# Kernel optimization log

Measured on AMD Instinct MI355X. Metric: run time of the kernel, lower is better.

Reference implementation:

```python
import jax, jax.numpy as jnp
import numpy as np

N, E, O, C, D_IN, OUT, L, B = 10000, 80000, 10, 64, 16, 16, 2, 16
DEG, WIDEN, BD = 3, 4, 64
EPS = 1e-6


def fibonacci_sphere(n):
    # deterministic near-uniform grid of n unit vectors on S^2 (stands in for GridGenerator's repulsion grid)
    i = jnp.arange(n, dtype=jnp.float32) + 0.5
    phi = jnp.arccos(1.0 - 2.0 * i / n)
    theta = jnp.pi * (1.0 + 5.0 ** 0.5) * i
    return jnp.stack([jnp.cos(theta) * jnp.sin(phi), jnp.sin(theta) * jnp.sin(phi), jnp.cos(phi)], axis=-1)


def poly_features(x, degree):
    # PolynomialFeatures: concat x, x(x)x, x(x)x(x)x, ... flattened outer products
    feats = [x]
    cur = x
    for _ in range(degree):
        cur = (cur[..., :, None] * x[..., None, :]).reshape(x.shape[:-1] + (-1,))
        feats.append(cur)
    return jnp.concatenate(feats, axis=-1)


def layer_norm(x, scale, bias):
    mu = jnp.mean(x, axis=-1, keepdims=True)
    var = jnp.mean((x - mu) ** 2, axis=-1, keepdims=True)
    return (x - mu) * jax.lax.rsqrt(var + EPS) * scale + bias


def setup_inputs():
    key = jax.random.key(0)
    ks = jax.random.split(key, 16)
    def w(k, shape):
        return jax.random.normal(k, shape, dtype=jnp.float32) / np.sqrt(shape[-2])
    P_SP = 2 + 4 + 8 + 16  # poly features of 2-dim spatial invariants, degree 3
    P_OR = 4               # poly features of 1-dim orientation invariant, degree 3
    return {
        "x": jax.random.normal(ks[0], (N, D_IN), jnp.float32),
        "pos": jax.random.normal(ks[1], (N, 3), jnp.float32),
        "basis_w1": w(ks[2], (P_SP, C)), "basis_b1": jnp.zeros((C,), jnp.float32),
        "basis_w2": w(ks[3], (C, BD)), "basis_b2": jnp.zeros((BD,), jnp.float32),
        "fbasis_w1": w(ks[4], (P_OR, C)), "fbasis_b1": jnp.zeros((C,), jnp.float32),
        "fbasis_w2": w(ks[5], (C, BD)), "fbasis_b2": jnp.zeros((BD,), jnp.float32),
        "embed_w": w(ks[6], (D_IN, C)),
        "conv_kw": w(ks[7], (L, BD, C)),
        "conv_fw": w(ks[8], (L, BD, C)),
        "conv_b": jnp.zeros((L, C), jnp.float32),
        "norm_s": jnp.ones((L, C), jnp.float32),
        "norm_b": jnp.zeros((L, C), jnp.float32),
        "lin1_w": w(ks[9], (L, C, WIDEN * C)), "lin1_b": jnp.zeros((L, WIDEN * C), jnp.float32),
        "lin2_w": w(ks[10], (L, WIDEN * C, C)), "lin2_b": jnp.zeros((L, C), jnp.float32),
        "ro_w": w(ks[11], (L, C, OUT)), "ro_b": jnp.zeros((L, OUT), jnp.float32),
        "edge_index": jax.random.randint(ks[12], (2, E), 0, N, jnp.int32),
        "batch": jnp.sort(jax.random.randint(ks[13], (N,), 0, B, jnp.int32)),
    }


def reference(x, pos, basis_w1, basis_b1, basis_w2, basis_b2, fbasis_w1, fbasis_b1, fbasis_w2, fbasis_b2, embed_w, conv_kw, conv_fw, conv_b, norm_s, norm_b, lin1_w, lin1_b, lin2_w, lin2_b, ro_w, ro_b, edge_index, batch):
    ori = fibonacci_sphere(O)                                             # [O,3]
    send, recv = edge_index[0], edge_index[1]
    rel = (pos[send] - pos[recv])[:, None, :]                              # [E,1,3]
    inv1 = jnp.sum(rel * ori[None], axis=-1, keepdims=True)                # [E,O,1]
    inv2 = jnp.linalg.norm(rel - inv1 * ori[None], axis=-1, keepdims=True) # [E,O,1]
    inv3 = jnp.sum(ori[None, :, :] * ori[:, None, :], axis=-1, keepdims=True)  # [O,O,1]
    sp = jnp.concatenate([inv1, inv2], axis=-1)                            # [E,O,2]
    kb = jax.nn.gelu(poly_features(sp, DEG) @ basis_w1 + basis_b1)
    kb = jax.nn.gelu(kb @ basis_w2 + basis_b2)                             # [E,O,BD]
    fkb = jax.nn.gelu(poly_features(inv3, DEG) @ fbasis_w1 + fbasis_b1)
    fkb = jax.nn.gelu(fkb @ fbasis_w2 + fbasis_b2)                         # [O,O,BD]
    h = jnp.broadcast_to((x @ embed_w)[:, None, :], (N, O, C))             # [N,O,C]
    readout = jnp.zeros((N, O, OUT), h.dtype)
    for l in range(L):
        # depthwise spatial conv: gather-send, modulate by kernel, scatter-add to receivers
        msg = h[send] * (kb @ conv_kw[l])                                  # [E,O,C]
        h1 = jax.ops.segment_sum(msg, recv, num_segments=N)                # [N,O,C]
        # depthwise fiber (orientation) conv
        fk = fkb @ conv_fw[l]                                              # [O,O,C]
        h2 = jnp.einsum('noc,poc->npc', h1, fk) / O + conv_b[l]
        # ConvNeXt MLP + residual
        y = layer_norm(h2, norm_s[l], norm_b[l])
        y = jax.nn.gelu(y @ lin1_w[l] + lin1_b[l]) @ lin2_w[l] + lin2_b[l]
        h = h + y
        readout = readout + (h @ ro_w[l] + ro_b[l])
    readout = readout / L
    out_scalar = jnp.mean(readout, axis=-2)                                # [N,OUT]
    pooled = jnp.zeros((B, OUT), out_scalar.dtype).at[batch].add(out_scalar)
    return pooled
```

## Files before the change

### kernel.cpp

```cpp
#include <hip/hip_runtime.h>
#include <math.h>

#define N_   10000
#define E_   80000
#define O_   10
#define B_   16
#define OUT_ 16
#define NROW_ (N_*O_)
#define NITEM_ (E_*O_)

typedef __attribute__((ext_vector_type(8))) short bf16x8;
typedef __attribute__((ext_vector_type(4))) short bf16x4;
typedef __attribute__((ext_vector_type(4))) float f32x4;

#define MFMA16(a,b,c) __builtin_amdgcn_mfma_f32_16x16x32_bf16(a,b,c,0,0,0)

__device__ __forceinline__ float gelu_f(float x) {
    float u = fmaf(0.044715f, x * x, 1.0f);
    float e = __builtin_amdgcn_exp2f(2.3022083f * x * u);
    float r = __builtin_amdgcn_rcpf(e + 1.0f);
    return fmaf(-x, r, x);
}

__device__ __forceinline__ unsigned short f2bf(float f) {
    union { float f; unsigned int u; } v; v.f = f;
    unsigned int r = v.u + 0x7FFFu + ((v.u >> 16) & 1u);
    return (unsigned short)(r >> 16);
}
__device__ __forceinline__ float bf2f(unsigned short u) {
    union { unsigned int u; float f; } v; v.u = ((unsigned int)u) << 16;
    return v.f;
}
__device__ __forceinline__ unsigned int cvtpk(float lo, float hi) {
    unsigned int r;
    asm("v_cvt_pk_bf16_f32 %0, %1, %2" : "=v"(r) : "v"(lo), "v"(hi));
    return r;
}
__device__ __forceinline__ bf16x4 pack4(float a, float b, float c, float d) {
    union { unsigned int u[2]; bf16x4 v; } z;
    z.u[0] = cvtpk(a, b);
    z.u[1] = cvtpk(c, d);
    return z.v;
}

__device__ __forceinline__ void fib_vec(int idx, float& vx, float& vy, float& vz) {
    float i = (float)idx + 0.5f;
    float phi = acosf(1.0f - 2.0f * i / (float)O_);
    float theta = 3.14159265358979323846f * (1.0f + 2.2360679774997896964f) * i;
    float sp = sinf(phi);
    vx = cosf(theta) * sp; vy = sinf(theta) * sp; vz = cosf(phi);
}

__global__ __launch_bounds__(256) void k_pack(
    const float* __restrict__ bw1, const float* __restrict__ bw2,
    const float* __restrict__ ckw, const float* __restrict__ l1w,
    const float* __restrict__ l2w, const float* __restrict__ row_w,
    float* __restrict__ orig,
    unsigned short* __restrict__ wW1P, unsigned short* __restrict__ wW2P,
    unsigned short* __restrict__ wCKP, unsigned short* __restrict__ wL1P,
    unsigned short* __restrict__ wL2P, unsigned short* __restrict__ wROP)
{
    const int g = blockIdx.x * 256 + threadIdx.x;
    if (g < 2048) {
        int idx = g;
        int t = idx >> 9, rem = idx & 511;
        int ln = rem >> 3, j = rem & 7;
        int row = t*16 + (ln & 15);
        int k = (ln >> 4)*8 + j;
        float s = 0.0f;
        if (k < 14) {
            const int moff[14] = {0,1,2,3,5,6,7,10,13,14,15,19,25,29};
            const int mcnt[14] = {1,1,1,2,1,1,3,3,1,1,4,6,4,1};
            const int mlist[30] = {0,1,2,3,4,5,6,7,8,10,9,11,12,13,14,
                                   15,16,18,22,17,19,20,23,24,26,21,25,27,28,29};
            for (int q = 0; q < mcnt[k]; ++q) s += bw1[mlist[moff[k]+q]*64 + row];
        }
        wW1P[idx] = f2bf(s);
    } else if (g < 6144) {
        int idx = g - 2048;
        int t = idx >> 9, rem = idx & 511;
        int mt = t >> 1, ks = t & 1;
        int ln = rem >> 3, j = rem & 7;
        int row = mt*16 + (ln & 15);
        int k = ks*32 + (ln >> 4)*8 + j;
        wW2P[idx] = f2bf(bw2[k*64 + row]);
    } else if (g < 14336) {
        int idx = g - 6144;
        int l = idx >> 12, r2 = idx & 4095;
        int t = r2 >> 9, rem = r2 & 511;
        int mt = t >> 1, ks = t & 1;
        int ln = rem >> 3, j = rem & 7;
        int row = mt*16 + (ln & 15);
        int k = ks*32 + (ln >> 4)*8 + j;
        wCKP[idx] = f2bf(ckw[l*4096 + k*64 + row]);
    } else if (g < 47104) {
        int idx = g - 14336;
        int l = idx >> 14, r2 = idx & 16383;
        int t = r2 >> 9, rem = r2 & 511;
        int mt = t >> 1, ks = t & 1;
        int ln = rem >> 3, j = rem & 7;
        int row = mt*16 + (ln & 15);
        int k = ks*32 + (ln >> 4)*8 + j;
        wL1P[idx] = f2bf(l1w[l*16384 + k*256 + row]);
    } else if (g < 79872) {
        int idx = g - 47104;
        int l = idx >> 14, r2 = idx & 16383;
        int t = r2 >> 9, rem = r2 & 511;
        int mt2 = t >> 3, ksg = t & 7;
        int ln = rem >> 3, j = rem & 7;
        int row = mt2*16 + (ln & 15);
        int k = ksg*32 + (ln >> 4)*8 + j;
        wL2P[idx] = f2bf(l2w[l*16384 + k*64 + row]);
    } else if (g < 81920) {
        int idx = g - 79872;
        int l = idx >> 10, r2 = idx & 1023;
        int ks = r2 >> 9, rem = r2 & 511;
        int ln = rem >> 3, j = rem & 7;
        int row = ln & 15;
        int k = ks*32 + (ln >> 4)*8 + j;
        wROP[idx] = f2bf(row_w[l*1024 + k*16 + row]);
    } else if (g < 81920 + O_) {
        int o = g - 81920;
        float vx, vy, vz;
        fib_vec(o, vx, vy, vz);
        orig[o*3+0] = vx; orig[o*3+1] = vy; orig[o*3+2] = vz;
    }
}

__global__ __launch_bounds__(256) void k_fibpre(
    const float* __restrict__ fw1, const float* __restrict__ fb1,
    const float* __restrict__ fw2, const float* __restrict__ fb2,
    const float* __restrict__ cfw, float* __restrict__ fkg)
{
    __shared__ float sRow[4][64];
    const int wv = threadIdx.x >> 6, lane = threadIdx.x & 63;
    const int pr = blockIdx.x * 4 + wv;
    if (pr >= 100) return;
    const int i = pr / O_, j = pr % O_;
    float ix, iy, iz, jx, jy, jz;
    fib_vec(i, ix, iy, iz);
    fib_vec(j, jx, jy, jz);
    float a = ix*jx + iy*jy + iz*jz;
    float a2 = a*a, a3 = a2*a, a4 = a3*a;
    float v = fb1[lane];
    v = fmaf(a,  fw1[0*64+lane], v);
    v = fmaf(a2, fw1[1*64+lane], v);
    v = fmaf(a3, fw1[2*64+lane], v);
    v = fmaf(a4, fw1[3*64+lane], v);
    sRow[wv][lane] = gelu_f(v);
    float acc = fb2[lane];
    for (int b = 0; b < 64; ++b) acc = fmaf(sRow[wv][b], fw2[b*64+lane], acc);
    sRow[wv][lane] = gelu_f(acc);
    for (int l = 0; l < 2; ++l) {
        float s = 0.0f;
        for (int b = 0; b < 64; ++b) s = fmaf(sRow[wv][b], cfw[l*4096 + b*64 + lane], s);
        fkg[l*6400 + pr*64 + lane] = s;
    }
}

__global__ __launch_bounds__(256) void k_embed(
    const float* __restrict__ x, const float* __restrict__ ew,
    float* __restrict__ hg, unsigned short* __restrict__ hbf0)
{
    int t = blockIdx.x * 256 + threadIdx.x;
    if (t >= N_ * 64) return;
    int n = t >> 6, c = t & 63;
    float v = 0.0f;
#pragma unroll
    for (int k = 0; k < 16; ++k) v = fmaf(x[n*16+k], ew[k*64+c], v);
    int base = n * 640 + c;
#pragma unroll
    for (int o = 0; o < O_; ++o) hg[base + o*64] = v;
    hbf0[t] = f2bf(v);
}

__global__ __launch_bounds__(256) void k_hist(const int* __restrict__ ei, int* __restrict__ counts)
{
    int e = blockIdx.x * 256 + threadIdx.x;
    if (e < E_) atomicAdd(&counts[ei[E_ + e]], 1);
}

__global__ __launch_bounds__(1024) void k_scan(
    const int* __restrict__ counts, int* __restrict__ offs, int* __restrict__ cursor)
{
    __shared__ int part[1024];
    int t = threadIdx.x;
    const int CH = 10;
    int base_i = t * CH;
    int s = 0;
#pragma unroll
    for (int i = 0; i < CH; ++i) { int idx = base_i + i; if (idx < N_) s += counts[idx]; }
    part[t] = s;
    __syncthreads();
    for (int off = 1; off < 1024; off <<= 1) {
        int v = (t >= off) ? part[t - off] : 0;
        __syncthreads();
        part[t] += v;
        __syncthreads();
    }
    int run = (t > 0) ? part[t - 1] : 0;
#pragma unroll
    for (int i = 0; i < CH; ++i) {
        int idx = base_i + i;
        if (idx < N_) { offs[idx] = run; cursor[idx] = run; run += counts[idx]; }
    }
    if (t == 1023) offs[N_] = run;
}

__global__ __launch_bounds__(256) void k_scatter(
    const int* __restrict__ ei, const float* __restrict__ pos,
    int* __restrict__ cursor, int* __restrict__ csend, int* __restrict__ crecv,
    float* __restrict__ crel)
{
    int e = blockIdx.x * 256 + threadIdx.x;
    if (e >= E_) return;
    int s = ei[e], r = ei[E_ + e];
    int slot = atomicAdd(&cursor[r], 1);
    csend[slot] = s;
    crecv[slot] = r;
    crel[slot*3+0] = pos[s*3+0] - pos[r*3+0];
    crel[slot*3+1] = pos[s*3+1] - pos[r*3+1];
    crel[slot*3+2] = pos[s*3+2] - pos[r*3+2];
}

template<int KS, bool BIAS, bool GELU>
__device__ __forceinline__ void mfma_stageP(
    unsigned short* sData, const unsigned short* __restrict__ Wp,
    const float* __restrict__ bias, int rbase, int lane)
{
    const int lm = lane & 15, lk = lane >> 4;
    bf16x8 Bf[4][KS];
#pragma unroll
    for (int nt = 0; nt < 4; ++nt)
#pragma unroll
        for (int ks = 0; ks < KS; ++ks) {
            int r = rbase + nt*16 + lm;
            int kb = ks*64 + lk*16;
            Bf[nt][ks] = *(const bf16x8*)((const char*)sData + r*128 + (kb ^ ((r&7)<<4)));
        }
#pragma unroll
    for (int mt = 0; mt < 4; ++mt) {
        bf16x8 Af[KS];
#pragma unroll
        for (int ks = 0; ks < KS; ++ks)
            Af[ks] = *(const bf16x8*)(Wp + ((mt*KS + ks)*64 + lane)*8);
        f32x4 b4 = {0,0,0,0};
        if (BIAS) b4 = *(const f32x4*)(bias + mt*16 + (lk<<2));
#pragma unroll
        for (int nt = 0; nt < 4; ++nt) {
            f32x4 acc = b4;
#pragma unroll
            for (int ks = 0; ks < KS; ++ks) acc = MFMA16(Af[ks], Bf[nt][ks], acc);
            float v0 = acc[0], v1 = acc[1], v2 = acc[2], v3 = acc[3];
            if (GELU) { v0 = gelu_f(v0); v1 = gelu_f(v1); v2 = gelu_f(v2); v3 = gelu_f(v3); }
            bf16x4 pk = pack4(v0, v1, v2, v3);
            int rr = rbase + nt*16 + lm;
            int cb = mt*32 + (lk<<3);
            *(bf16x4*)((char*)sData + rr*128 + (cb ^ ((rr&7)<<4))) = pk;
        }
    }
}

template<bool L0>
__global__ __launch_bounds__(128) void k_msg(
    const unsigned short* __restrict__ hbf, float* __restrict__ h1g,
    const int* __restrict__ csend, const int* __restrict__ crecv,
    const float* __restrict__ crel, const float* __restrict__ ori,
    const unsigned short* __restrict__ wW1P, const unsigned short* __restrict__ wW2P,
    const unsigned short* __restrict__ wCKP_l,
    const float* __restrict__ bb1, const float* __restrict__ bb2)
{
    __shared__ unsigned short sData[128*64];
    const int tid = threadIdx.x;
    const int lane = tid & 63, wv = tid >> 6;
    const int item = blockIdx.x * 128 + tid;
    const int slot = item / 10;
    const int oo = item - slot * 10;
    const int snd = csend[slot];
    const int rcv = crecv[slot];
    {
        float r0 = crel[slot*3+0], r1 = crel[slot*3+1], r2 = crel[slot*3+2];
        float o0 = ori[oo*3+0], o1 = ori[oo*3+1], o2 = ori[oo*3+2];
        float a = r0*o0 + r1*o1 + r2*o2;
        float p0 = fmaf(-a, o0, r0), p1 = fmaf(-a, o1, r1), p2 = fmaf(-a, o2, r2);
        float b = sqrtf(p0*p0 + p1*p1 + p2*p2);
        float a2 = a*a, b2 = b*b, ab = a*b;
        float m[14];
        m[0]=a; m[1]=b; m[2]=a2; m[3]=ab; m[4]=b2;
        m[5]=a2*a; m[6]=a2*b; m[7]=a*b2; m[8]=b2*b;
        m[9]=a2*a2; m[10]=a2*ab; m[11]=a2*b2; m[12]=ab*b2; m[13]=b2*b2;
        unsigned int pk[16];
#pragma unroll
        for (int j = 0; j < 7; ++j) pk[j] = cvtpk(m[2*j], m[2*j+1]);
#pragma unroll
        for (int j = 7; j < 16; ++j) pk[j] = 0;
        int r = tid;
#pragma unroll
        for (int q = 0; q < 4; ++q) {
            int cb = q*16;
            *(f32x4*)((char*)sData + r*128 + (cb ^ ((r&7)<<4))) = ((const f32x4*)pk)[q];
        }
    }
    const int rbase = wv * 64;
    mfma_stageP<1, true,  true >(sData, wW1P,   bb1, rbase, lane);
    mfma_stageP<2, true,  true >(sData, wW2P,   bb2, rbase, lane);
    mfma_stageP<2, false, false>(sData, wCKP_l, (const float*)0, rbase, lane);

    const int myaddr = L0 ? (snd * 64) : ((snd * 10 + oo) * 64);
    int prevr = __shfl_up(rcv, 1);
    unsigned long long bmask = __ballot(lane > 0 && rcv != prevr);
    const unsigned short* hb = hbf + lane;
    float a0=0,a1c=0,a2c=0,a3c=0,a4c=0,a5c=0,a6c=0,a7c=0,a8c=0,a9c=0;
    int cur = __builtin_amdgcn_readfirstlane(rcv);
    int soi = (blockIdx.x * 128 + rbase) % 10;
#define FLUSH_RUN(R) { float* bp = h1g + (R)*640 + lane; \
    atomicAdd(bp+0,a0); atomicAdd(bp+64,a1c); atomicAdd(bp+128,a2c); atomicAdd(bp+192,a3c); \
    atomicAdd(bp+256,a4c); atomicAdd(bp+320,a5c); atomicAdd(bp+384,a6c); atomicAdd(bp+448,a7c); \
    atomicAdd(bp+512,a8c); atomicAdd(bp+576,a9c); \
    a0=a1c=a2c=a3c=a4c=a5c=a6c=a7c=a8c=a9c=0.0f; }
#pragma unroll
    for (int ch = 0; ch < 4; ++ch) {
        unsigned short hvu[16];
        float kcv[16];
#pragma unroll
        for (int j = 0; j < 16; ++j) {
            const int i = ch*16 + j;
            hvu[j] = hb[__builtin_amdgcn_readlane(myaddr, i)];
            const int rr = rbase + i;
            kcv[j] = bf2f(*(const unsigned short*)((const char*)sData + rr*128 + ((lane*2) ^ ((rr&7)<<4))));
        }
#pragma unroll
        for (int j = 0; j < 16; ++j) {
            const int i = ch*16 + j;
            if (bmask & (1ull << i)) { FLUSH_RUN(cur); cur = __builtin_amdgcn_readlane(rcv, i); }
            float mv = kcv[j] * bf2f(hvu[j]);
            if      (soi == 0) a0  += mv;
            else if (soi == 1) a1c += mv;
            else if (soi == 2) a2c += mv;
            else if (soi == 3) a3c += mv;
            else if (soi == 4) a4c += mv;
            else if (soi == 5) a5c += mv;
            else if (soi == 6) a6c += mv;
            else if (soi == 7) a7c += mv;
            else if (soi == 8) a8c += mv;
            else               a9c += mv;
            soi = (soi == 9) ? 0 : soi + 1;
        }
    }
    FLUSH_RUN(cur);
#undef FLUSH_RUN
}

__global__ __launch_bounds__(256) void k_fln(
    const float* __restrict__ h1, const float* __restrict__ fkg,
    const float* __restrict__ cb, const float* __restrict__ ns,
    const float* __restrict__ nb, unsigned short* __restrict__ y)
{
    __shared__ float sFK[6400];
    const int tid = threadIdx.x;
    for (int i = tid; i < 6400; i += 256) sFK[i] = fkg[i];
    __syncthreads();
    const int lane = tid & 63, wv = tid >> 6;
    float cbv = cb[lane], nsv = ns[lane], nbv = nb[lane];
    for (int g4 = blockIdx.x; g4 < N_/4; g4 += gridDim.x) {
        const int n = g4 * 4 + wv;
        float hr[10];
#pragma unroll
        for (int o = 0; o < O_; ++o) hr[o] = h1[n*640 + o*64 + lane];
#pragma unroll
        for (int p = 0; p < O_; ++p) {
            float v = 0.0f;
#pragma unroll
            for (int o = 0; o < O_; ++o) v = fmaf(hr[o], sFK[(p*O_+o)*64 + lane], v);
            v = v * 0.1f + cbv;
            float s = v, q = v*v;
#pragma unroll
            for (int d = 1; d < 64; d <<= 1) { s += __shfl_xor(s, d); q += __shfl_xor(q, d); }
            float mu = s * (1.0f/64.0f);
            float var = q * (1.0f/64.0f) - mu*mu;
            float rs = rsqrtf(var + 1e-6f);
            float yv = (v - mu) * rs * nsv + nbv;
            y[(n*O_ + p)*64 + lane] = f2bf(yv);
        }
    }
}

__global__ __launch_bounds__(256, 4) void k_mlp(
    unsigned short* ybuf, float* __restrict__ hg, float* __restrict__ rout,
    const unsigned short* __restrict__ wL1P_l, const float* __restrict__ l1b_l,
    const unsigned short* __restrict__ wL2P_l, const float* __restrict__ l2b_l,
    const unsigned short* __restrict__ wROP_l, const float* __restrict__ rob_l)
{
    __shared__ unsigned short sA[64*64];
    const int tid = threadIdx.x;
    const int lane = tid & 63, wv = tid >> 6;
    const int rb = blockIdx.x * 64;
#pragma unroll
    for (int i = tid*16; i < 64*128; i += 256*16) {
        int r = i >> 7, off = i & 127;
        int grow = rb + r; if (grow >= NROW_) grow = NROW_ - 1;
        *(f32x4*)((char*)sA + r*128 + (off ^ ((r&7)<<4))) =
            *(const f32x4*)((const char*)ybuf + (size_t)grow*128 + off);
    }
    __syncthreads();
    const int lm = lane & 15, lk = lane >> 4;
    const int r0 = wv*16 + lm;
    bf16x8 Yf[2];
#pragma unroll
    for (int ks = 0; ks < 2; ++ks) {
        int kb = ks*64 + lk*16;
        Yf[ks] = *(const bf16x8*)((const char*)sA + r0*128 + (kb ^ ((r0&7)<<4)));
    }
    f32x4 acc2[4];
#pragma unroll
    for (int m = 0; m < 4; ++m) acc2[m] = *(const f32x4*)(l2b_l + m*16 + (lk<<2));
#pragma unroll
    for (int jb = 0; jb < 4; ++jb) {
#pragma unroll
        for (int mt = 0; mt < 4; ++mt) {
            bf16x8 A1[2];
#pragma unroll
            for (int ks = 0; ks < 2; ++ks)
                A1[ks] = *(const bf16x8*)(wL1P_l + (((jb*4 + mt)*2 + ks)*64 + lane)*8);
            f32x4 acc = *(const f32x4*)(l1b_l + jb*64 + mt*16 + (lk<<2));
            acc = MFMA16(A1[0], Yf[0], acc);
            acc = MFMA16(A1[1], Yf[1], acc);
            bf16x4 pk = pack4(gelu_f(acc[0]), gelu_f(acc[1]), gelu_f(acc[2]), gelu_f(acc[3]));
            int cb = mt*32 + (lk<<3);
            *(bf16x4*)((char*)sA + r0*128 + (cb ^ ((r0&7)<<4))) = pk;
        }
        bf16x8 Mf[2];
#pragma unroll
        for (int ks = 0; ks < 2; ++ks) {
            int kb = ks*64 + lk*16;
            Mf[ks] = *(const bf16x8*)((const char*)sA + r0*128 + (kb ^ ((r0&7)<<4)));
        }
#pragma unroll
        for (int mt2 = 0; mt2 < 4; ++mt2) {
            bf16x8 A2[2];
#pragma unroll
            for (int ks = 0; ks < 2; ++ks)
                A2[ks] = *(const bf16x8*)(wL2P_l + ((mt2*8 + jb*2 + ks)*64 + lane)*8);
            acc2[mt2] = MFMA16(A2[0], Mf[0], acc2[mt2]);
            acc2[mt2] = MFMA16(A2[1], Mf[1], acc2[mt2]);
        }
    }
    const int grow = rb + r0;
    const bool valid = grow < NROW_;
    const int growc = valid ? grow : (NROW_ - 1);
#pragma unroll
    for (int mt2 = 0; mt2 < 4; ++mt2) {
        f32x4 hv = *(const f32x4*)(hg + (size_t)growc*64 + mt2*16 + (lk<<2));
        f32x4 hn;
#pragma unroll
        for (int r = 0; r < 4; ++r) hn[r] = hv[r] + acc2[mt2][r];
        bf16x4 pk = pack4(hn[0], hn[1], hn[2], hn[3]);
        if (valid) {
            *(f32x4*)(hg + (size_t)grow*64 + mt2*16 + (lk<<2)) = hn;
            *(bf16x4*)((char*)ybuf + (size_t)grow*128 + (mt2*16 + (lk<<2))*2) = pk;
        }
        int cb = mt2*32 + (lk<<3);
        *(bf16x4*)((char*)sA + r0*128 + (cb ^ ((r0&7)<<4))) = pk;
    }
    bf16x8 Ro[2];
#pragma unroll
    for (int ks = 0; ks < 2; ++ks)
        Ro[ks] = *(const bf16x8*)(wROP_l + (ks*64 + lane)*8);
    f32x4 r4 = *(const f32x4*)(rob_l + (lk<<2));
    bf16x8 Hf[2];
#pragma unroll
    for (int ks = 0; ks < 2; ++ks) {
        int kb = ks*64 + lk*16;
        Hf[ks] = *(const bf16x8*)((const char*)sA + r0*128 + (kb ^ ((r0&7)<<4)));
    }
    r4 = MFMA16(Ro[0], Hf[0], r4);
    r4 = MFMA16(Ro[1], Hf[1], r4);
    if (valid) *(f32x4*)(rout + (size_t)grow*16 + (lk<<2)) = r4;
}

__global__ __launch_bounds__(256) void k_pool(
    const float* __restrict__ r0, const float* __restrict__ r1,
    const int* __restrict__ batch, float* __restrict__ out)
{
    int t = blockIdx.x * 256 + threadIdx.x;
    if (t >= N_ * 16) return;
    int n = t >> 4, j = t & 15;
    float s = 0.0f;
#pragma unroll
    for (int p = 0; p < O_; ++p)
        s += r0[(n*O_ + p)*16 + j] + r1[(n*O_ + p)*16 + j];
    atomicAdd(&out[batch[n]*16 + j], s * (1.0f/20.0f));
}

extern "C" void kernel_launch(void* const* d_in, const int* in_sizes, int n_in,
                              void* d_out, int out_size, void* d_ws, size_t ws_size,
                              hipStream_t stream)
{
    const float* x    = (const float*)d_in[0];
    const float* pos  = (const float*)d_in[1];
    const float* bw1  = (const float*)d_in[2];
    const float* bb1  = (const float*)d_in[3];
    const float* bw2  = (const float*)d_in[4];
    const float* bb2  = (const float*)d_in[5];
    const float* fw1  = (const float*)d_in[6];
    const float* fb1  = (const float*)d_in[7];
    const float* fw2  = (const float*)d_in[8];
    const float* fb2  = (const float*)d_in[9];
    const float* embw = (const float*)d_in[10];
    const float* ckw  = (const float*)d_in[11];
    const float* cfw  = (const float*)d_in[12];
    const float* cb   = (const float*)d_in[13];
    const float* ns   = (const float*)d_in[14];
    const float* nbp  = (const float*)d_in[15];
    const float* l1w  = (const float*)d_in[16];
    const float* l1b  = (const float*)d_in[17];
    const float* l2w  = (const float*)d_in[18];
    const float* l2b  = (const float*)d_in[19];
    const float* row  = (const float*)d_in[20];
    const float* rob  = (const float*)d_in[21];
    const int*   ei   = (const int*)d_in[22];
    const int*   batch= (const int*)d_in[23];
    float* out = (float*)d_out;

    char* w = (char*)d_ws;
    size_t off = 0;
    auto alloc = [&](size_t bytes) -> char* {
        char* p = w + off; off += (bytes + 255) / 256 * 256; return p;
    };
    float* ori    = (float*)alloc(32 * 4);
    float* fkg    = (float*)alloc(2 * 6400 * 4);
    unsigned short* wW1P = (unsigned short*)alloc(4*512*2);
    unsigned short* wW2P = (unsigned short*)alloc(8*512*2);
    unsigned short* wCKP = (unsigned short*)alloc(2*8*512*2);
    unsigned short* wL1P = (unsigned short*)alloc(2*32*512*2);
    unsigned short* wL2P = (unsigned short*)alloc(2*32*512*2);
    unsigned short* wROP = (unsigned short*)alloc(2*2*512*2);
    float* h      = (float*)alloc((size_t)N_ * 640 * 4);
    float* h1     = (float*)alloc((size_t)N_ * 640 * 4);
    unsigned short* y = (unsigned short*)alloc((size_t)NROW_ * 64 * 2);
    unsigned short* hbf0 = (unsigned short*)alloc((size_t)N_ * 64 * 2);
    float* rout0  = (float*)alloc((size_t)NROW_ * 16 * 4);
    float* rout1  = (float*)alloc((size_t)NROW_ * 16 * 4);
    float* crel   = (float*)alloc((size_t)E_ * 3 * 4);
    int*   counts = (int*)alloc((N_ + 1) * 4);
    int*   offs   = (int*)alloc((N_ + 1) * 4);
    int*   cursor = (int*)alloc((N_ + 1) * 4);
    int*   csend  = (int*)alloc((size_t)E_ * 4);
    int*   crecv  = (int*)alloc((size_t)E_ * 4);

    hipMemsetAsync(out, 0, (size_t)out_size * 4, stream);
    hipMemsetAsync(counts, 0, (N_ + 1) * 4, stream);

    k_pack<<<321, 256, 0, stream>>>(bw1, bw2, ckw, l1w, l2w, row, ori,
                                    wW1P, wW2P, wCKP, wL1P, wL2P, wROP);
    k_fibpre<<<25, 256, 0, stream>>>(fw1, fb1, fw2, fb2, cfw, fkg);
    k_embed<<<(N_ * 64 + 255) / 256, 256, 0, stream>>>(x, embw, h, hbf0);
    k_hist<<<(E_ + 255) / 256, 256, 0, stream>>>(ei, counts);
    k_scan<<<1, 1024, 0, stream>>>(counts, offs, cursor);
    k_scatter<<<(E_ + 255) / 256, 256, 0, stream>>>(ei, pos, cursor, csend, crecv, crel);

    for (int l = 0; l < 2; ++l) {
        hipMemsetAsync(h1, 0, (size_t)N_ * 640 * 4, stream);
        if (l == 0)
            k_msg<true><<<NITEM_ / 128, 128, 0, stream>>>(hbf0, h1, csend, crecv, crel, ori,
                                                          wW1P, wW2P, wCKP + l*4096, bb1, bb2);
        else
            k_msg<false><<<NITEM_ / 128, 128, 0, stream>>>(y, h1, csend, crecv, crel, ori,
                                                           wW1P, wW2P, wCKP + l*4096, bb1, bb2);
        k_fln<<<625, 256, 0, stream>>>(h1, fkg + l*6400, cb + l*64, ns + l*64, nbp + l*64, y);
        k_mlp<<<(NROW_ + 63) / 64, 256, 0, stream>>>(y, h, (l == 0 ? rout0 : rout1),
                                                     wL1P + l*16384, l1b + l*256,
                                                     wL2P + l*16384, l2b + l*64,
                                                     wROP + l*1024, rob + l*16);
    }
    k_pool<<<(N_ * 16 + 255) / 256, 256, 0, stream>>>(rout0, rout1, batch, out);
}
```

Baseline: 432.7 us.

## Compute both layers' edge kernels once in layer 0 and reuse in layer 1

```diff
diff --git a/kernel.cpp b/kernel.cpp
--- a/kernel.cpp
+++ b/kernel.cpp
@@ -223,21 +223,27 @@
     crel[slot*3+2] = pos[s*3+2] - pos[r*3+2];
 }
 
-template<int KS, bool BIAS, bool GELU>
-__device__ __forceinline__ void mfma_stageP(
-    unsigned short* sData, const unsigned short* __restrict__ Wp,
-    const float* __restrict__ bias, int rbase, int lane)
+template<int KS>
+__device__ __forceinline__ void loadB(
+    const unsigned short* sData, int lane, bf16x8 Bf[4][KS])
 {
     const int lm = lane & 15, lk = lane >> 4;
-    bf16x8 Bf[4][KS];
 #pragma unroll
     for (int nt = 0; nt < 4; ++nt)
 #pragma unroll
         for (int ks = 0; ks < KS; ++ks) {
-            int r = rbase + nt*16 + lm;
+            int r = nt*16 + lm;
             int kb = ks*64 + lk*16;
             Bf[nt][ks] = *(const bf16x8*)((const char*)sData + r*128 + (kb ^ ((r&7)<<4)));
         }
+}
+
+template<int KS, bool BIAS, bool GELU>
+__device__ __forceinline__ void stageC(
+    unsigned short* sData, const bf16x8 Bf[4][KS],
+    const unsigned short* __restrict__ Wp, const float* __restrict__ bias, int lane)
+{
+    const int lm = lane & 15, lk = lane >> 4;
 #pragma unroll
     for (int mt = 0; mt < 4; ++mt) {
         bf16x8 Af[KS];
@@ -254,15 +260,82 @@
             float v0 = acc[0], v1 = acc[1], v2 = acc[2], v3 = acc[3];
             if (GELU) { v0 = gelu_f(v0); v1 = gelu_f(v1); v2 = gelu_f(v2); v3 = gelu_f(v3); }
             bf16x4 pk = pack4(v0, v1, v2, v3);
-            int rr = rbase + nt*16 + lm;
+            int rr = nt*16 + lm;
             int cb = mt*32 + (lk<<3);
             *(bf16x4*)((char*)sData + rr*128 + (cb ^ ((rr&7)<<4))) = pk;
         }
     }
 }
 
+__device__ __forceinline__ void phase0(
+    unsigned short* sData, int slot, int oo, const float* __restrict__ crel,
+    const float* __restrict__ ori, int tid)
+{
+    float r0 = crel[slot*3+0], r1 = crel[slot*3+1], r2 = crel[slot*3+2];
+    float o0 = ori[oo*3+0], o1 = ori[oo*3+1], o2 = ori[oo*3+2];
+    float a = r0*o0 + r1*o1 + r2*o2;
+    float p0 = fmaf(-a, o0, r0), p1 = fmaf(-a, o1, r1), p2 = fmaf(-a, o2, r2);
+    float b = sqrtf(p0*p0 + p1*p1 + p2*p2);
+    float a2 = a*a, b2 = b*b, ab = a*b;
+    float m[14];
+    m[0]=a; m[1]=b; m[2]=a2; m[3]=ab; m[4]=b2;
+    m[5]=a2*a; m[6]=a2*b; m[7]=a*b2; m[8]=b2*b;
+    m[9]=a2*a2; m[10]=a2*ab; m[11]=a2*b2; m[12]=ab*b2; m[13]=b2*b2;
+    unsigned int pk[16];
+#pragma unroll
+    for (int j = 0; j < 7; ++j) pk[j] = cvtpk(m[2*j], m[2*j+1]);
+#pragma unroll
+    for (int j = 7; j < 16; ++j) pk[j] = 0;
+#pragma unroll
+    for (int q = 0; q < 4; ++q) {
+        int cb = q*16;
+        *(f32x4*)((char*)sData + tid*128 + (cb ^ ((tid&7)<<4))) = ((const f32x4*)pk)[q];
+    }
+}
+
+#define SCATTER_BODY(KC_EXPR)                                                        \
+    int prevr = __shfl_up(rcv, 1);                                                   \
+    unsigned long long bmask = __ballot(lane > 0 && rcv != prevr);                   \
+    float a0=0,a1c=0,a2c=0,a3c=0,a4c=0,a5c=0,a6c=0,a7c=0,a8c=0,a9c=0;                \
+    int cur = __builtin_amdgcn_readfirstlane(rcv);                                   \
+    int soi = item0 % 10;                                                            \
+    _Pragma("unroll")                                                                \
+    for (int ch = 0; ch < 4; ++ch) {                                                 \
+        unsigned short hvu[16]; float kcv[16];                                       \
+        _Pragma("unroll")                                                            \
+        for (int j = 0; j < 16; ++j) {                                               \
+            const int i = ch*16 + j;                                                 \
+            hvu[j] = hb[__builtin_amdgcn_readlane(myaddr, i)];                       \
+            kcv[j] = (KC_EXPR);                                                      \
+        }                                                                            \
+        _Pragma("unroll")                                                            \
+        for (int j = 0; j < 16; ++j) {                                               \
+            const int i = ch*16 + j;                                                 \
+            if (bmask & (1ull << i)) { FLUSH_RUN(cur); cur = __builtin_amdgcn_readlane(rcv, i); } \
+            float mv = kcv[j] * bf2f(hvu[j]);                                        \
+            if      (soi == 0) a0  += mv;                                            \
+            else if (soi == 1) a1c += mv;                                            \
+            else if (soi == 2) a2c += mv;                                            \
+            else if (soi == 3) a3c += mv;                                            \
+            else if (soi == 4) a4c += mv;                                            \
+            else if (soi == 5) a5c += mv;                                            \
+            else if (soi == 6) a6c += mv;                                            \
+            else if (soi == 7) a7c += mv;                                            \
+            else if (soi == 8) a8c += mv;                                            \
+            else               a9c += mv;                                            \
+            soi = (soi == 9) ? 0 : soi + 1;                                          \
+        }                                                                            \
+    }                                                                                \
+    FLUSH_RUN(cur);
+
+#define FLUSH_RUN(R) { float* bp = h1g + (R)*640 + lane; \
+    atomicAdd(bp+0,a0); atomicAdd(bp+64,a1c); atomicAdd(bp+128,a2c); atomicAdd(bp+192,a3c); \
+    atomicAdd(bp+256,a4c); atomicAdd(bp+320,a5c); atomicAdd(bp+384,a6c); atomicAdd(bp+448,a7c); \
+    atomicAdd(bp+512,a8c); atomicAdd(bp+576,a9c); \
+    a0=a1c=a2c=a3c=a4c=a5c=a6c=a7c=a8c=a9c=0.0f; }
+
 template<bool L0>
-__global__ __launch_bounds__(128) void k_msg(
+__global__ __launch_bounds__(64) void k_msg(
     const unsigned short* __restrict__ hbf, float* __restrict__ h1g,
     const int* __restrict__ csend, const int* __restrict__ crecv,
     const float* __restrict__ crel, const float* __restrict__ ori,
@@ -270,91 +343,95 @@
     const unsigned short* __restrict__ wCKP_l,
     const float* __restrict__ bb1, const float* __restrict__ bb2)
 {
-    __shared__ unsigned short sData[128*64];
-    const int tid = threadIdx.x;
-    const int lane = tid & 63, wv = tid >> 6;
-    const int item = blockIdx.x * 128 + tid;
+    __shared__ unsigned short sData[64*64];
+    const int lane = threadIdx.x;
+    const int item0 = blockIdx.x * 64;
+    const int item = item0 + lane;
     const int slot = item / 10;
     const int oo = item - slot * 10;
     const int snd = csend[slot];
     const int rcv = crecv[slot];
+    phase0(sData, slot, oo, crel, ori, lane);
     {
-        float r0 = crel[slot*3+0], r1 = crel[slot*3+1], r2 = crel[slot*3+2];
-        float o0 = ori[oo*3+0], o1 = ori[oo*3+1], o2 = ori[oo*3+2];
-        float a = r0*o0 + r1*o1 + r2*o2;
-        float p0 = fmaf(-a, o0, r0), p1 = fmaf(-a, o1, r1), p2 = fmaf(-a, o2, r2);
-        float b = sqrtf(p0*p0 + p1*p1 + p2*p2);
-        float a2 = a*a, b2 = b*b, ab = a*b;
-        float m[14];
-        m[0]=a; m[1]=b; m[2]=a2; m[3]=ab; m[4]=b2;
-        m[5]=a2*a; m[6]=a2*b; m[7]=a*b2; m[8]=b2*b;
-        m[9]=a2*a2; m[10]=a2*ab; m[11]=a2*b2; m[12]=ab*b2; m[13]=b2*b2;
-        unsigned int pk[16];
-#pragma unroll
-        for (int j = 0; j < 7; ++j) pk[j] = cvtpk(m[2*j], m[2*j+1]);
-#pragma unroll
-        for (int j = 7; j < 16; ++j) pk[j] = 0;
-        int r = tid;
-#pragma unroll
-        for (int q = 0; q < 4; ++q) {
-            int cb = q*16;
-            *(f32x4*)((char*)sData + r*128 + (cb ^ ((r&7)<<4))) = ((const f32x4*)pk)[q];
-        }
-    }
-    const int rbase = wv * 64;
-    mfma_stageP<1, true,  true >(sData, wW1P,   bb1, rbase, lane);
-    mfma_stageP<2, true,  true >(sData, wW2P,   bb2, rbase, lane);
-    mfma_stageP<2, false, false>(sData, wCKP_l, (const float*)0, rbase, lane);
-
+        bf16x8 Bf1[4][1]; loadB<1>(sData, lane, Bf1);
+        stageC<1, true, true>(sData, Bf1, wW1P, bb1, lane);
+    }
+    {
+        bf16x8 Bf2[4][2]; loadB<2>(sData, lane, Bf2);
+        stageC<2, true, true>(sData, Bf2, wW2P, bb2, lane);
+    }
+    {
+        bf16x8 Bf3[4][2]; loadB<2>(sData, lane, Bf3);
+        stageC<2, false, false>(sData, Bf3, wCKP_l, (const float*)0, lane);
+    }
     const int myaddr = L0 ? (snd * 64) : ((snd * 10 + oo) * 64);
-    int prevr = __shfl_up(rcv, 1);
-    unsigned long long bmask = __ballot(lane > 0 && rcv != prevr);
     const unsigned short* hb = hbf + lane;
-    float a0=0,a1c=0,a2c=0,a3c=0,a4c=0,a5c=0,a6c=0,a7c=0,a8c=0,a9c=0;
-    int cur = __builtin_amdgcn_readfirstlane(rcv);
-    int soi = (blockIdx.x * 128 + rbase) % 10;
-#define FLUSH_RUN(R) { float* bp = h1g + (R)*640 + lane; \
-    atomicAdd(bp+0,a0); atomicAdd(bp+64,a1c); atomicAdd(bp+128,a2c); atomicAdd(bp+192,a3c); \
-    atomicAdd(bp+256,a4c); atomicAdd(bp+320,a5c); atomicAdd(bp+384,a6c); atomicAdd(bp+448,a7c); \
-    atomicAdd(bp+512,a8c); atomicAdd(bp+576,a9c); \
-    a0=a1c=a2c=a3c=a4c=a5c=a6c=a7c=a8c=a9c=0.0f; }
-#pragma unroll
-    for (int ch = 0; ch < 4; ++ch) {
-        unsigned short hvu[16];
-        float kcv[16];
-#pragma unroll
-        for (int j = 0; j < 16; ++j) {
-            const int i = ch*16 + j;
-            hvu[j] = hb[__builtin_amdgcn_readlane(myaddr, i)];
-            const int rr = rbase + i;
-            kcv[j] = bf2f(*(const unsigned short*)((const char*)sData + rr*128 + ((lane*2) ^ ((rr&7)<<4))));
-        }
-#pragma unroll
-        for (int j = 0; j < 16; ++j) {
-            const int i = ch*16 + j;
-            if (bmask & (1ull << i)) { FLUSH_RUN(cur); cur = __builtin_amdgcn_readlane(rcv, i); }
-            float mv = kcv[j] * bf2f(hvu[j]);
-            if      (soi == 0) a0  += mv;
-            else if (soi == 1) a1c += mv;
-            else if (soi == 2) a2c += mv;
-            else if (soi == 3) a3c += mv;
-            else if (soi == 4) a4c += mv;
-            else if (soi == 5) a5c += mv;
-            else if (soi == 6) a6c += mv;
-            else if (soi == 7) a7c += mv;
-            else if (soi == 8) a8c += mv;
-            else               a9c += mv;
-            soi = (soi == 9) ? 0 : soi + 1;
-        }
-    }
-    FLUSH_RUN(cur);
+    SCATTER_BODY(bf2f(*(const unsigned short*)((const char*)sData + i*128 + ((lane*2) ^ ((i&7)<<4)))))
+}
+
+__global__ __launch_bounds__(64) void k_msg0dual(
+    const unsigned short* __restrict__ hbf, float* __restrict__ h1g,
+    unsigned short* __restrict__ kc1g,
+    const int* __restrict__ csend, const int* __restrict__ crecv,
+    const float* __restrict__ crel, const float* __restrict__ ori,
+    const unsigned short* __restrict__ wW1P, const unsigned short* __restrict__ wW2P,
+    const unsigned short* __restrict__ wCK0, const unsigned short* __restrict__ wCK1,
+    const float* __restrict__ bb1, const float* __restrict__ bb2)
+{
+    __shared__ unsigned short sData[64*64];
+    const int lane = threadIdx.x;
+    const int item0 = blockIdx.x * 64;
+    const int item = item0 + lane;
+    const int slot = item / 10;
+    const int oo = item - slot * 10;
+    const int snd = csend[slot];
+    const int rcv = crecv[slot];
+    phase0(sData, slot, oo, crel, ori, lane);
+    {
+        bf16x8 Bf1[4][1]; loadB<1>(sData, lane, Bf1);
+        stageC<1, true, true>(sData, Bf1, wW1P, bb1, lane);
+    }
+    {
+        bf16x8 Bf2[4][2]; loadB<2>(sData, lane, Bf2);
+        stageC<2, true, true>(sData, Bf2, wW2P, bb2, lane);
+    }
+    bf16x8 Bf3[4][2]; loadB<2>(sData, lane, Bf3);
+    stageC<2, false, false>(sData, Bf3, wCK1, (const float*)0, lane);
+#pragma unroll
+    for (int q = 0; q < 8; ++q) {
+        f32x4 v = *(const f32x4*)((const char*)sData + lane*128 + ((q*16) ^ ((lane&7)<<4)));
+        *(f32x4*)((char*)kc1g + (size_t)item*128 + ((q*16) ^ ((lane&7)<<4))) = v;
+    }
+    stageC<2, false, false>(sData, Bf3, wCK0, (const float*)0, lane);
+    const int myaddr = snd * 64;
+    const unsigned short* hb = hbf + lane;
+    SCATTER_BODY(bf2f(*(const unsigned short*)((const char*)sData + i*128 + ((lane*2) ^ ((i&7)<<4)))))
+}
+
+__global__ __launch_bounds__(64) void k_msg1lite(
+    const unsigned short* __restrict__ kc1g, const unsigned short* __restrict__ hbf,
+    float* __restrict__ h1g,
+    const int* __restrict__ csend, const int* __restrict__ crecv)
+{
+    const int lane = threadIdx.x;
+    const int item0 = blockIdx.x * 64;
+    const int item = item0 + lane;
+    const int slot = item / 10;
+    const int oo = item - slot * 10;
+    const int snd = csend[slot];
+    const int rcv = crecv[slot];
+    const int myaddr = (snd * 10 + oo) * 64;
+    const unsigned short* hb = hbf + lane;
+    const char* kb = (const char*)kc1g + (size_t)item0 * 128;
+    SCATTER_BODY(bf2f(*(const unsigned short*)(kb + (size_t)i*128 + ((lane*2) ^ ((i&7)<<4)))))
+}
 #undef FLUSH_RUN
-}
+#undef SCATTER_BODY
 
 __global__ __launch_bounds__(256) void k_fln(
-    const float* __restrict__ h1, const float* __restrict__ fkg,
+    float* __restrict__ h1, const float* __restrict__ fkg,
     const float* __restrict__ cb, const float* __restrict__ ns,
-    const float* __restrict__ nb, unsigned short* __restrict__ y)
+    const float* __restrict__ nb, unsigned short* __restrict__ y, int zero_h1)
 {
     __shared__ float sFK[6400];
     const int tid = threadIdx.x;
@@ -367,6 +444,10 @@
         float hr[10];
 #pragma unroll
         for (int o = 0; o < O_; ++o) hr[o] = h1[n*640 + o*64 + lane];
+        if (zero_h1) {
+#pragma unroll
+            for (int o = 0; o < O_; ++o) h1[n*640 + o*64 + lane] = 0.0f;
+        }
 #pragma unroll
         for (int p = 0; p < O_; ++p) {
             float v = 0.0f;
@@ -547,7 +628,11 @@
     int*   cursor = (int*)alloc((N_ + 1) * 4);
     int*   csend  = (int*)alloc((size_t)E_ * 4);
     int*   crecv  = (int*)alloc((size_t)E_ * 4);
-
+    unsigned short* kc1g = nullptr;
+    if (ws_size >= off + (size_t)NITEM_ * 64 * 2 + 256)
+        kc1g = (unsigned short*)alloc((size_t)NITEM_ * 64 * 2);
+
+    hipMemsetAsync(h1, 0, (size_t)N_ * 640 * 4, stream);
     hipMemsetAsync(out, 0, (size_t)out_size * 4, stream);
     hipMemsetAsync(counts, 0, (N_ + 1) * 4, stream);
 
@@ -560,14 +645,23 @@
     k_scatter<<<(E_ + 255) / 256, 256, 0, stream>>>(ei, pos, cursor, csend, crecv, crel);
 
     for (int l = 0; l < 2; ++l) {
-        hipMemsetAsync(h1, 0, (size_t)N_ * 640 * 4, stream);
-        if (l == 0)
-            k_msg<true><<<NITEM_ / 128, 128, 0, stream>>>(hbf0, h1, csend, crecv, crel, ori,
-                                                          wW1P, wW2P, wCKP + l*4096, bb1, bb2);
-        else
-            k_msg<false><<<NITEM_ / 128, 128, 0, stream>>>(y, h1, csend, crecv, crel, ori,
-                                                           wW1P, wW2P, wCKP + l*4096, bb1, bb2);
-        k_fln<<<625, 256, 0, stream>>>(h1, fkg + l*6400, cb + l*64, ns + l*64, nbp + l*64, y);
+        if (l == 0) {
+            if (kc1g)
+                k_msg0dual<<<NITEM_ / 64, 64, 0, stream>>>(hbf0, h1, kc1g, csend, crecv,
+                                                           crel, ori, wW1P, wW2P,
+                                                           wCKP, wCKP + 4096, bb1, bb2);
+            else
+                k_msg<true><<<NITEM_ / 64, 64, 0, stream>>>(hbf0, h1, csend, crecv, crel, ori,
+                                                            wW1P, wW2P, wCKP, bb1, bb2);
+        } else {
+            if (kc1g)
+                k_msg1lite<<<NITEM_ / 64, 64, 0, stream>>>(kc1g, y, h1, csend, crecv);
+            else
+                k_msg<false><<<NITEM_ / 64, 64, 0, stream>>>(y, h1, csend, crecv, crel, ori,
+                                                             wW1P, wW2P, wCKP + 4096, bb1, bb2);
+        }
+        k_fln<<<625, 256, 0, stream>>>(h1, fkg + l*6400, cb + l*64, ns + l*64, nbp + l*64, y,
+                                       (l == 0) ? 1 : 0);
         k_mlp<<<(NROW_ + 63) / 64, 256, 0, stream>>>(y, h, (l == 0 ? rout0 : rout1),
                                                      wL1P + l*16384, l1b + l*256,
                                                      wL2P + l*16384, l2b + l*64,
```

After: 414.9 us. -4.1%, faster.
